# Kernel tuning notes

Hardware: AMD Instinct MI355X
Metric: run time of the kernel (lower is better)

The kernel has to match this reference:

```python
import jax, jax.numpy as jnp
import numpy as np

K = 3          # kernel_size
N = K * K      # sampling points per pixel
STRIDE = 1
PAD = 1
DIL = 1


def _conv2d(x, w, b):
    # standard NCHW conv for offset / modulation branches
    y = jax.lax.conv_general_dilated(
        x, w, window_strides=(STRIDE, STRIDE),
        padding=((PAD, PAD), (PAD, PAD)),
        rhs_dilation=(DIL, DIL),
        dimension_numbers=('NCHW', 'OIHW', 'NCHW'))
    return y + b[None, :, None, None]


def setup_inputs() -> dict:
    key = jax.random.key(0)
    ks = jax.random.split(key, 6)
    B, C, H, W, O = 8, 64, 96, 96, 64
    x = jax.random.normal(ks[0], (B, C, H, W), jnp.float32)
    # small random offset/modulation weights so sampling points are off-grid
    offset_w = jax.random.normal(ks[1], (2 * N, C, K, K), jnp.float32) * 0.01
    offset_b = jax.random.normal(ks[2], (2 * N,), jnp.float32) * 0.1
    m_w = jax.random.normal(ks[3], (N, C, K, K), jnp.float32) * 0.01
    m_b = jnp.zeros((N,), jnp.float32)
    # Conv3d(in=C, out=O, kernel=(1,1,N)) weight squeezed to [O, C, N]
    conv_w = jax.random.normal(ks[4], (O, C, N), jnp.float32) * (2.0 / (C * N)) ** 0.5
    conv_b = jnp.zeros((O,), jnp.float32)
    return dict(x=x, offset_w=offset_w, offset_b=offset_b,
                m_w=m_w, m_b=m_b, conv_w=conv_w, conv_b=conv_b)


def _deform_forward(x, offset_w, offset_b, m_w, m_b, conv_w, conv_b):
    B, C, H, W = x.shape
    offset = _conv2d(x, offset_w, offset_b)           # [B, 2n, h, w]
    m = jax.nn.sigmoid(_conv2d(x, m_w, m_b))          # [B, n, h, w]
    xp = jnp.pad(x, ((0, 0), (0, 0), (PAD, PAD), (PAD, PAD)))
    Hp, Wp = xp.shape[2], xp.shape[3]
    off = jnp.transpose(offset, (0, 2, 3, 1))         # [B, h, w, 2n]
    mod = jnp.transpose(m, (0, 2, 3, 1))              # [B, h, w, n]

    # p0: conv-center grid on the padded input; pn: kernel-tap offsets
    st = ((K - 1) // 2) * DIL
    p0_x = jnp.arange(st, Hp - (K // 2) * DIL, STRIDE, dtype=jnp.float32)  # [h]
    p0_y = jnp.arange(st, Wp - (K // 2) * DIL, STRIDE, dtype=jnp.float32)  # [w]
    r = jnp.arange(-((K - 1) // 2) * DIL, (K // 2) * DIL + 1, DIL, dtype=jnp.float32)
    pn_x, pn_y = jnp.meshgrid(r, r, indexing='ij')
    pn_x, pn_y = pn_x.reshape(N), pn_y.reshape(N)

    p_x = off[..., :N] + p0_x[None, :, None, None] + pn_x  # [B, h, w, n]
    p_y = off[..., N:] + p0_y[None, None, :, None] + pn_y

    fl_x = jnp.floor(jax.lax.stop_gradient(p_x))
    fl_y = jnp.floor(jax.lax.stop_gradient(p_y))
    q_tl_x = jnp.clip(fl_x, 0, Hp - 1).astype(jnp.int32)
    q_tl_y = jnp.clip(fl_y, 0, Wp - 1).astype(jnp.int32)
    q_br_x = jnp.clip(fl_x + 1, 0, Hp - 1).astype(jnp.int32)
    q_br_y = jnp.clip(fl_y + 1, 0, Wp - 1).astype(jnp.int32)

    pcx = jnp.clip(p_x, 0, Hp - 1)
    pcy = jnp.clip(p_y, 0, Wp - 1)

    tlx = q_tl_x.astype(pcx.dtype); tly = q_tl_y.astype(pcy.dtype)
    brx = q_br_x.astype(pcx.dtype); bry = q_br_y.astype(pcy.dtype)
    g_tl = (1 + (tlx - pcx)) * (1 + (tly - pcy))
    g_tr = (1 + (tlx - pcx)) * (1 - (bry - pcy))
    g_bl = (1 - (brx - pcx)) * (1 + (tly - pcy))
    g_br = (1 - (brx - pcx)) * (1 - (bry - pcy))

    xflat = xp.reshape(B, C, Hp * Wp)

    def gather(qx, qy):
        # per-batch gather: xf [C, Hp*Wp], idx [h, w, n] -> [C, h, w, n]
        return jax.vmap(lambda xf, i: xf[:, i])(xflat, qx * Wp + qy)

    xq_tl = gather(q_tl_x, q_tl_y)
    xq_tr = gather(q_tl_x, q_br_y)
    xq_bl = gather(q_br_x, q_tl_y)
    xq_br = gather(q_br_x, q_br_y)

    x_p = (g_tl[:, None] * xq_tl + g_tr[:, None] * xq_tr +
           g_bl[:, None] * xq_bl + g_br[:, None] * xq_br)
    x_p = x_p * mod[:, None]                           # modulation

    # Conv3d with (1,1,N) kernel == contraction over (C, N)
    out = jnp.einsum('bchwn,ocn->bohw', x_p, conv_w) + conv_b[None, :, None, None]
    return out


def reference(x, offset_w, offset_b, m_w, m_b, conv_w, conv_b):
    return _deform_forward(x, offset_w, offset_b, m_w, m_b, conv_w, conv_b)
```

## Files before the change

kernel.cpp:

```cpp
#include <hip/hip_runtime.h>
#include <hip/hip_fp16.h>
#include <cstddef>

#define B_   8
#define H_   96
#define W_   96
#define HW_  9216
#define PIX_ 73728

#define NWR    6
#define NWC    38
#define WINPX  228
#define NSLOTS 19

typedef __attribute__((ext_vector_type(8))) _Float16 halfx8;
typedef __attribute__((ext_vector_type(2))) __fp16 fp16x2_raw;
typedef __attribute__((ext_vector_type(4))) float floatx4;

#define XT_OFF   0
#define WFM_OFF  (XT_OFF + PIX_*64*2)
#define WFO_OFF  (WFM_OFF + 18*4*64*8*2)
#define WZ_OFF   (WFO_OFF + 18*2*64*8*2)

__device__ __forceinline__ unsigned pk2h(float a, float b) {
    fp16x2_raw h = __builtin_amdgcn_cvt_pkrtz(a, b);
    union { fp16x2_raw h2; unsigned u; } t; t.h2 = h; return t.u;
}
__device__ __forceinline__ halfx8 uph8(uint4 u) {
    union { uint4 u4; halfx8 h; } t; t.u4 = u; return t.h;
}
__device__ __forceinline__ halfx8 splat8(unsigned d) {
    union { unsigned u[4]; halfx8 h; } t;
    t.u[0] = d; t.u[1] = d; t.u[2] = d; t.u[3] = d; return t.h;
}
__device__ __forceinline__ void async_ld16(const void* g, void* l) {
    __builtin_amdgcn_global_load_lds((const __attribute__((address_space(1))) void*)g,
                                     (__attribute__((address_space(3))) void*)l,
                                     16, 0, 0);
}

__global__ __launch_bounds__(256) void k_transpose(const float* __restrict__ x,
                                                   unsigned short* __restrict__ xt,
                                                   const float* __restrict__ offw,
                                                   const float* __restrict__ mw,
                                                   const float* __restrict__ convw,
                                                   unsigned short* __restrict__ wfm,
                                                   unsigned short* __restrict__ wfo,
                                                   unsigned short* __restrict__ wz) {
    if (blockIdx.x >= 1152) {
        int g = (blockIdx.x - 1152) * 256 + threadIdx.x;
        if (g < 4608) {
            int lane = g & 63, mtks = g >> 6;
            int mt = mtks & 3, ks = mtks >> 2;
            int o = mt * 16 + (lane & 15), quad = lane >> 4;
            float v[8];
            #pragma unroll
            for (int j = 0; j < 8; ++j) {
                int k = ks * 32 + quad * 8 + j;
                int t = k / 64, c = k % 64;
                v[j] = convw[(size_t)(o * 64 + c) * 9 + t];
            }
            uint4 pk;
            pk.x = pk2h(v[0], v[1]); pk.y = pk2h(v[2], v[3]);
            pk.z = pk2h(v[4], v[5]); pk.w = pk2h(v[6], v[7]);
            *(uint4*)(wfm + (size_t)g * 8) = pk;
        } else if (g < 4608 + 2304) {
            int g2 = g - 4608;
            int lane = g2 & 63, mtks = g2 >> 6;
            int mt = mtks & 1, ks = mtks >> 1;
            int m = mt * 16 + (lane & 15), quad = lane >> 4;
            float v[8];
            #pragma unroll
            for (int j = 0; j < 8; ++j) {
                int k = ks * 32 + quad * 8 + j;
                int t = k / 64, c = k % 64;
                float f = 0.f;
                if (m < 18)      f = offw[(size_t)(m * 64 + c) * 9 + t];
                else if (m < 27) f = mw[(size_t)((m - 18) * 64 + c) * 9 + t];
                v[j] = f;
            }
            uint4 pk;
            pk.x = pk2h(v[0], v[1]); pk.y = pk2h(v[2], v[3]);
            pk.z = pk2h(v[4], v[5]); pk.w = pk2h(v[6], v[7]);
            *(uint4*)(wfo + (size_t)g2 * 8) = pk;
        } else if (g < 4608 + 2304 + 8) {
            uint4 z = make_uint4(0, 0, 0, 0);
            *(uint4*)(wz + (size_t)(g - 6912) * 8) = z;
        }
        return;
    }

    __shared__ float tile[64 * 65];
    int bb  = blockIdx.x / 144;
    int sp0 = (blockIdx.x % 144) * 64;
    int t = threadIdx.x;
    int s4 = (t & 15) * 4, cq = t >> 4;
    #pragma unroll
    for (int i = 0; i < 4; ++i) {
        int c = cq + 16 * i;
        float4 v = *(const float4*)&x[(size_t)(bb * 64 + c) * HW_ + sp0 + s4];
        tile[c * 65 + s4 + 0] = v.x;
        tile[c * 65 + s4 + 1] = v.y;
        tile[c * 65 + s4 + 2] = v.z;
        tile[c * 65 + s4 + 3] = v.w;
    }
    __syncthreads();
    int c8 = t & 7, sgrp = t >> 3;
    #pragma unroll
    for (int i = 0; i < 2; ++i) {
        int s2 = i * 32 + sgrp;
        uint4 pk;
        pk.x = pk2h(tile[(c8 * 8 + 0) * 65 + s2], tile[(c8 * 8 + 1) * 65 + s2]);
        pk.y = pk2h(tile[(c8 * 8 + 2) * 65 + s2], tile[(c8 * 8 + 3) * 65 + s2]);
        pk.z = pk2h(tile[(c8 * 8 + 4) * 65 + s2], tile[(c8 * 8 + 5) * 65 + s2]);
        pk.w = pk2h(tile[(c8 * 8 + 6) * 65 + s2], tile[(c8 * 8 + 7) * 65 + s2]);
        *(uint4*)(xt + (size_t)(bb * HW_ + sp0 + s2) * 64 + c8 * 8) = pk;
    }
}

__global__ __launch_bounds__(256, 4) void k_fused(const unsigned short* __restrict__ xt,
                                                  const unsigned short* __restrict__ wfo,
                                                  const unsigned short* __restrict__ wfm,
                                                  const float* __restrict__ offb,
                                                  const float* __restrict__ mb,
                                                  const float* __restrict__ convb,
                                                  const unsigned short* __restrict__ wz,
                                                  float* __restrict__ out) {
    __shared__ __align__(16) unsigned char s_win[(WINPX + NSLOTS) * 128];
    __shared__ __align__(16) unsigned char s_u[9216];
    __shared__ int s_cnt;
    float* s_off = (float*)s_u;
    unsigned char* s_meta = s_u;

    int tid = threadIdx.x;
    int w = tid >> 6, lane = tid & 63, col = lane & 15, quad = lane >> 4;
    int blk = (blockIdx.x & 7) * 144 + (blockIdx.x >> 3);
    int bb  = blk / 144;
    int rem = blk % 144;
    int hr  = (rem / 3) * 2;
    int wc  = (rem % 3) * 32;
    const unsigned short* xtb = xt + (size_t)bb * HW_ * 64;

    if (tid == 0) s_cnt = 0;
    {
        int p0  = lane >> 3;
        int cgx = (lane & 7) ^ p0;
        const unsigned short* wzp = wz + cgx * 8;
        for (int i = w; i < 29; i += 4) {
            int p = i * 8 + p0;
            int wr = p / NWC, wcl = p - wr * NWC;
            int gr = hr - 2 + wr, gc = wc - 3 + wcl;
            bool ok = (p < WINPX) && ((unsigned)gr < 96u) && ((unsigned)gc < 96u);
            const unsigned short* src = ok ? (xtb + ((size_t)(gr * 96 + gc) * 64 + cgx * 8)) : wzp;
            async_ld16(src, s_win + i * 1024);
        }
    }
    __syncthreads();

    floatx4 aoff0 = (floatx4){0.f, 0.f, 0.f, 0.f};
    floatx4 aoff1 = (floatx4){0.f, 0.f, 0.f, 0.f};
    {
        int wr_base = 2 + (w >> 1);
        int wc_base = 3 + (w & 1) * 16 + col;
        #pragma unroll
        for (int t = 0; t < 9; ++t) {
            int dh = t / 3 - 1, dw = t % 3 - 1;
            int p = (wr_base + dh) * NWC + (wc_base + dw);
            int pb = p << 7, psw = (p & 7) << 4;
            #pragma unroll
            for (int ksl = 0; ksl < 2; ++ksl) {
                int ks = t * 2 + ksl;
                halfx8 a0 = *(const halfx8*)(wfo + ((size_t)(ks * 2 + 0) * 64 + lane) * 8);
                halfx8 a1 = *(const halfx8*)(wfo + ((size_t)(ks * 2 + 1) * 64 + lane) * 8);
                uint4 bvu = *(const uint4*)(s_win + pb + ((quad * 16 + ksl * 64) ^ psw));
                halfx8 bv = uph8(bvu);
                aoff0 = __builtin_amdgcn_mfma_f32_16x16x32_f16(a0, bv, aoff0, 0, 0, 0);
                aoff1 = __builtin_amdgcn_mfma_f32_16x16x32_f16(a1, bv, aoff1, 0, 0, 0);
            }
        }
    }
    #pragma unroll
    for (int r = 0; r < 4; ++r) {
        s_off[(quad * 4 + r) * 66 + (w * 16 + col)] = aoff0[r];
        int m = 16 + quad * 4 + r;
        if (m < 27) s_off[m * 66 + (w * 16 + col)] = aoff1[r];
    }
    __syncthreads();

    float ox0, oy0, mv0, ox1, oy1, mv1, ox2 = 0.f, oy2 = 0.f, mv2 = 0.f;
    bool has2 = (tid + 512) < 576;
    {
        int px = tid & 63, n = tid >> 6;
        ox0 = s_off[n * 66 + px]        + offb[n];
        oy0 = s_off[(9 + n) * 66 + px]  + offb[9 + n];
        mv0 = s_off[(18 + n) * 66 + px] + mb[n];
    }
    {
        int id = tid + 256;
        int px = id & 63, n = id >> 6;
        ox1 = s_off[n * 66 + px]        + offb[n];
        oy1 = s_off[(9 + n) * 66 + px]  + offb[9 + n];
        mv1 = s_off[(18 + n) * 66 + px] + mb[n];
    }
    if (has2) {
        int id = tid + 512;
        int px = id & 63, n = id >> 6;
        ox2 = s_off[n * 66 + px]        + offb[n];
        oy2 = s_off[(9 + n) * 66 + px]  + offb[9 + n];
        mv2 = s_off[(18 + n) * 66 + px] + mb[n];
    }
    __syncthreads();

    auto meta_one = [&](int id, float ox, float oy, float mv) {
        int px = id & 63, n = id >> 6;
        float modv = 1.f / (1.f + __expf(-mv));
        int prow = hr + (px >> 5), pcol = wc + (px & 31);
        float pxx = ox + (float)(prow + 1) + (float)(n / 3 - 1);
        float pyy = oy + (float)(pcol + 1) + (float)(n % 3 - 1);
        float flx = floorf(pxx), fly = floorf(pyy);
        float tlxf = fminf(fmaxf(flx,       0.f), 97.f);
        float tlyf = fminf(fmaxf(fly,       0.f), 97.f);
        float brxf = fminf(fmaxf(flx + 1.f, 0.f), 97.f);
        float bryf = fminf(fmaxf(fly + 1.f, 0.f), 97.f);
        float pcx  = fminf(fmaxf(pxx, 0.f), 97.f);
        float pcy  = fminf(fmaxf(pyy, 0.f), 97.f);
        float gx0 = 1.f + tlxf - pcx;
        float gx1 = 1.f - (brxf - pcx);
        float gy0 = 1.f + tlyf - pcy;
        float gy1 = 1.f - (bryf - pcy);
        int tlx = (int)tlxf, tly = (int)tlyf, brx = (int)brxf, bry = (int)bryf;
        int   qxs[4] = {tlx, tlx, brx, brx};
        int   qys[4] = {tly, bry, tly, bry};
        float gs4[4] = {gx0 * gy0, gx0 * gy1, gx1 * gy0, gx1 * gy1};
        unsigned short si[4]; unsigned short hg[4];
        #pragma unroll
        for (int c4 = 0; c4 < 4; ++c4) {
            int qx = qxs[c4], qy = qys[c4];
            bool valid = (qx >= 1) && (qx <= 96) && (qy >= 1) && (qy <= 96);
            int gr = qx - 1, gc = qy - 1;
            int wr = gr - (hr - 2), wcl = gc - (wc - 3);
            bool inwin = ((unsigned)wr < (unsigned)NWR) && ((unsigned)wcl < (unsigned)NWC);
            unsigned short idxv; float gvf;
            if (inwin) {
                idxv = (unsigned short)(wr * NWC + wcl);
                gvf = gs4[c4] * modv;
            } else if (!valid) {
                idxv = 0; gvf = 0.f;
            } else {
                int s = atomicAdd(&s_cnt, 1);
                int gidx = gr * 96 + gc;
                if (s < NSLOTS) {
                    int ps = WINPX + s;
                    #pragma unroll
                    for (int ch = 0; ch < 8; ++ch) {
                        uint4 v = *(const uint4*)(xtb + (size_t)gidx * 64 + ch * 8);
                        *(uint4*)(s_win + (size_t)ps * 128 + ((ch ^ (ps & 7)) * 16)) = v;
                    }
                    idxv = (unsigned short)ps;
                } else {
                    idxv = (unsigned short)(0x8000u | (unsigned)gidx);
                }
                gvf = gs4[c4] * modv;
            }
            si[c4] = idxv;
            hg[c4] = __half_as_ushort(__float2half_rn(gvf));
        }
        uint4 mw4;
        mw4.x = si[0] | ((unsigned)si[1] << 16);
        mw4.y = si[2] | ((unsigned)si[3] << 16);
        mw4.z = hg[0] | ((unsigned)hg[1] << 16);
        mw4.w = hg[2] | ((unsigned)hg[3] << 16);
        *(uint4*)(s_meta + ((size_t)px * 9 + n) * 16) = mw4;
    };
    meta_one(tid,       ox0, oy0, mv0);
    meta_one(tid + 256, ox1, oy1, mv1);
    if (has2) meta_one(tid + 512, ox2, oy2, mv2);
    __syncthreads();

    int mth = w & 1, pg = w >> 1;
    floatx4 acc[2][2];
    #pragma unroll
    for (int jj = 0; jj < 2; ++jj)
        #pragma unroll
        for (int mtl = 0; mtl < 2; ++mtl) acc[jj][mtl] = (floatx4){0.f, 0.f, 0.f, 0.f};

    int qk0 = quad * 16, qk1 = quad * 16 + 64;

    #pragma unroll
    for (int n = 0; n < 9; ++n) {
        halfx8 af00 = *(const halfx8*)(wfm + ((size_t)((n * 2 + 0) * 4 + mth * 2 + 0) * 64 + lane) * 8);
        halfx8 af01 = *(const halfx8*)(wfm + ((size_t)((n * 2 + 0) * 4 + mth * 2 + 1) * 64 + lane) * 8);
        halfx8 af10 = *(const halfx8*)(wfm + ((size_t)((n * 2 + 1) * 4 + mth * 2 + 0) * 64 + lane) * 8);
        halfx8 af11 = *(const halfx8*)(wfm + ((size_t)((n * 2 + 1) * 4 + mth * 2 + 1) * 64 + lane) * 8);
        #pragma unroll
        for (int jj = 0; jj < 2; ++jj) {
            int px = pg * 32 + jj * 16 + col;
            uint4 mu = *(const uint4*)(s_meta + ((size_t)px * 9 + n) * 16);
            unsigned i0 = mu.x & 0xFFFFu, i1 = mu.x >> 16;
            unsigned i2 = mu.y & 0xFFFFu, i3 = mu.y >> 16;
            int pm0 = (i0 & 0x8000u) ? 0 : (int)i0;
            int pm1 = (i1 & 0x8000u) ? 0 : (int)i1;
            int pm2 = (i2 & 0x8000u) ? 0 : (int)i2;
            int pm3 = (i3 & 0x8000u) ? 0 : (int)i3;
            int b0 = pm0 << 7, s0 = (pm0 & 7) << 4;
            int b1 = pm1 << 7, s1 = (pm1 & 7) << 4;
            int b2 = pm2 << 7, s2 = (pm2 & 7) << 4;
            int b3 = pm3 << 7, s3 = (pm3 & 7) << 4;
            uint4 cA0 = *(const uint4*)(s_win + b0 + (qk0 ^ s0));
            uint4 cA1 = *(const uint4*)(s_win + b1 + (qk0 ^ s1));
            uint4 cA2 = *(const uint4*)(s_win + b2 + (qk0 ^ s2));
            uint4 cA3 = *(const uint4*)(s_win + b3 + (qk0 ^ s3));
            uint4 cB0 = *(const uint4*)(s_win + b0 + (qk1 ^ s0));
            uint4 cB1 = *(const uint4*)(s_win + b1 + (qk1 ^ s1));
            uint4 cB2 = *(const uint4*)(s_win + b2 + (qk1 ^ s2));
            uint4 cB3 = *(const uint4*)(s_win + b3 + (qk1 ^ s3));
            if (__any((int)((i0 | i1 | i2 | i3) & 0x8000u))) {
                if (i0 & 0x8000u) { size_t ga = (size_t)(i0 & 0x3FFFu) * 64 + quad * 8;
                    cA0 = *(const uint4*)(xtb + ga); cB0 = *(const uint4*)(xtb + ga + 32); }
                if (i1 & 0x8000u) { size_t ga = (size_t)(i1 & 0x3FFFu) * 64 + quad * 8;
                    cA1 = *(const uint4*)(xtb + ga); cB1 = *(const uint4*)(xtb + ga + 32); }
                if (i2 & 0x8000u) { size_t ga = (size_t)(i2 & 0x3FFFu) * 64 + quad * 8;
                    cA2 = *(const uint4*)(xtb + ga); cB2 = *(const uint4*)(xtb + ga + 32); }
                if (i3 & 0x8000u) { size_t ga = (size_t)(i3 & 0x3FFFu) * 64 + quad * 8;
                    cA3 = *(const uint4*)(xtb + ga); cB3 = *(const uint4*)(xtb + ga + 32); }
            }
            unsigned gl0 = (mu.z & 0xFFFFu) | (mu.z << 16);
            unsigned gl1 = (mu.z >> 16) | (mu.z & 0xFFFF0000u);
            unsigned gl2 = (mu.w & 0xFFFFu) | (mu.w << 16);
            unsigned gl3 = (mu.w >> 16) | (mu.w & 0xFFFF0000u);
            halfx8 g0 = splat8(gl0), g1 = splat8(gl1), g2 = splat8(gl2), g3 = splat8(gl3);
            halfx8 vA = uph8(cA0) * g0;
            vA += uph8(cA1) * g1; vA += uph8(cA2) * g2; vA += uph8(cA3) * g3;
            halfx8 vB = uph8(cB0) * g0;
            vB += uph8(cB1) * g1; vB += uph8(cB2) * g2; vB += uph8(cB3) * g3;
            acc[jj][0] = __builtin_amdgcn_mfma_f32_16x16x32_f16(af00, vA, acc[jj][0], 0, 0, 0);
            acc[jj][1] = __builtin_amdgcn_mfma_f32_16x16x32_f16(af01, vA, acc[jj][1], 0, 0, 0);
            acc[jj][0] = __builtin_amdgcn_mfma_f32_16x16x32_f16(af10, vB, acc[jj][0], 0, 0, 0);
            acc[jj][1] = __builtin_amdgcn_mfma_f32_16x16x32_f16(af11, vB, acc[jj][1], 0, 0, 0);
        }
    }

    int prow = hr + pg;
    #pragma unroll
    for (int mtl = 0; mtl < 2; ++mtl) {
        float4 cb4 = *(const float4*)&convb[mth * 32 + mtl * 16 + quad * 4];
        #pragma unroll
        for (int jj = 0; jj < 2; ++jj) {
            int sp = prow * 96 + wc + jj * 16 + col;
            #pragma unroll
            for (int r = 0; r < 4; ++r) {
                int o = mth * 32 + mtl * 16 + quad * 4 + r;
                float bias = (r == 0) ? cb4.x : (r == 1) ? cb4.y : (r == 2) ? cb4.z : cb4.w;
                out[(size_t)(bb * 64 + o) * HW_ + sp] = acc[jj][mtl][r] + bias;
            }
        }
    }
}

extern "C" void kernel_launch(void* const* d_in, const int* in_sizes, int n_in,
                              void* d_out, int out_size, void* d_ws, size_t ws_size,
                              hipStream_t stream) {
    const float* x     = (const float*)d_in[0];
    const float* offw  = (const float*)d_in[1];
    const float* offb  = (const float*)d_in[2];
    const float* mw    = (const float*)d_in[3];
    const float* mb    = (const float*)d_in[4];
    const float* convw = (const float*)d_in[5];
    const float* convb = (const float*)d_in[6];
    char* ws = (char*)d_ws;
    unsigned short* xt16 = (unsigned short*)(ws + XT_OFF);
    unsigned short* wfm  = (unsigned short*)(ws + WFM_OFF);
    unsigned short* wfo  = (unsigned short*)(ws + WFO_OFF);
    unsigned short* wz   = (unsigned short*)(ws + WZ_OFF);
    float* out = (float*)d_out;

    k_transpose<<<dim3(1152 + 28), dim3(256), 0, stream>>>(x, xt16, offw, mw, convw, wfm, wfo, wz);
    k_fused    <<<dim3(1152),      dim3(256), 0, stream>>>(xt16, wfo, wfm, offb, mb, convb, wz, out);
}
```

Measured before the change: 113.3 us.

## Remap warp tiling so each wave samples 16 pixels once and covers all 64 outputs

Warps previously split output channels in two halves, so each pixel's bilinear gather and interpolation from LDS was done twice, once per wave of a pair. Now each wave owns 16 distinct pixels and computes all four output-channel tiles, so every sample is gathered and interpolated exactly once. The cost is loading twice as many weight fragments per wave per tap, from global/L1, and wider dependency chains on four accumulators.

```diff
diff --git a/kernel.cpp b/kernel.cpp
--- a/kernel.cpp
+++ b/kernel.cpp
@@ -277,82 +277,71 @@
     if (has2) meta_one(tid + 512, ox2, oy2, mv2);
     __syncthreads();
 
-    int mth = w & 1, pg = w >> 1;
-    floatx4 acc[2][2];
-    #pragma unroll
-    for (int jj = 0; jj < 2; ++jj)
+    int px3 = (w >> 1) * 32 + (w & 1) * 16 + col;
+    floatx4 acc[4];
+    #pragma unroll
+    for (int mt = 0; mt < 4; ++mt) acc[mt] = (floatx4){0.f, 0.f, 0.f, 0.f};
+
+    int qk0 = quad * 16, qk1 = quad * 16 + 64;
+
+    #pragma unroll
+    for (int n = 0; n < 9; ++n) {
+        uint4 mu = *(const uint4*)(s_meta + ((size_t)px3 * 9 + n) * 16);
+        unsigned i0 = mu.x & 0xFFFFu, i1 = mu.x >> 16;
+        unsigned i2 = mu.y & 0xFFFFu, i3 = mu.y >> 16;
+        int pm0 = (i0 & 0x8000u) ? 0 : (int)i0;
+        int pm1 = (i1 & 0x8000u) ? 0 : (int)i1;
+        int pm2 = (i2 & 0x8000u) ? 0 : (int)i2;
+        int pm3 = (i3 & 0x8000u) ? 0 : (int)i3;
+        int b0 = pm0 << 7, s0 = (pm0 & 7) << 4;
+        int b1 = pm1 << 7, s1 = (pm1 & 7) << 4;
+        int b2 = pm2 << 7, s2 = (pm2 & 7) << 4;
+        int b3 = pm3 << 7, s3 = (pm3 & 7) << 4;
+        uint4 cA0 = *(const uint4*)(s_win + b0 + (qk0 ^ s0));
+        uint4 cA1 = *(const uint4*)(s_win + b1 + (qk0 ^ s1));
+        uint4 cA2 = *(const uint4*)(s_win + b2 + (qk0 ^ s2));
+        uint4 cA3 = *(const uint4*)(s_win + b3 + (qk0 ^ s3));
+        uint4 cB0 = *(const uint4*)(s_win + b0 + (qk1 ^ s0));
+        uint4 cB1 = *(const uint4*)(s_win + b1 + (qk1 ^ s1));
+        uint4 cB2 = *(const uint4*)(s_win + b2 + (qk1 ^ s2));
+        uint4 cB3 = *(const uint4*)(s_win + b3 + (qk1 ^ s3));
+        if (__any((int)((i0 | i1 | i2 | i3) & 0x8000u))) {
+            if (i0 & 0x8000u) { size_t ga = (size_t)(i0 & 0x3FFFu) * 64 + quad * 8;
+                cA0 = *(const uint4*)(xtb + ga); cB0 = *(const uint4*)(xtb + ga + 32); }
+            if (i1 & 0x8000u) { size_t ga = (size_t)(i1 & 0x3FFFu) * 64 + quad * 8;
+                cA1 = *(const uint4*)(xtb + ga); cB1 = *(const uint4*)(xtb + ga + 32); }
+            if (i2 & 0x8000u) { size_t ga = (size_t)(i2 & 0x3FFFu) * 64 + quad * 8;
+                cA2 = *(const uint4*)(xtb + ga); cB2 = *(const uint4*)(xtb + ga + 32); }
+            if (i3 & 0x8000u) { size_t ga = (size_t)(i3 & 0x3FFFu) * 64 + quad * 8;
+                cA3 = *(const uint4*)(xtb + ga); cB3 = *(const uint4*)(xtb + ga + 32); }
+        }
+        unsigned gl0 = (mu.z & 0xFFFFu) | (mu.z << 16);
+        unsigned gl1 = (mu.z >> 16) | (mu.z & 0xFFFF0000u);
+        unsigned gl2 = (mu.w & 0xFFFFu) | (mu.w << 16);
+        unsigned gl3 = (mu.w >> 16) | (mu.w & 0xFFFF0000u);
+        halfx8 g0 = splat8(gl0), g1 = splat8(gl1), g2 = splat8(gl2), g3 = splat8(gl3);
+        halfx8 vA = uph8(cA0) * g0;
+        vA += uph8(cA1) * g1; vA += uph8(cA2) * g2; vA += uph8(cA3) * g3;
+        halfx8 vB = uph8(cB0) * g0;
+        vB += uph8(cB1) * g1; vB += uph8(cB2) * g2; vB += uph8(cB3) * g3;
         #pragma unroll
-        for (int mtl = 0; mtl < 2; ++mtl) acc[jj][mtl] = (floatx4){0.f, 0.f, 0.f, 0.f};
-
-    int qk0 = quad * 16, qk1 = quad * 16 + 64;
-
-    #pragma unroll
-    for (int n = 0; n < 9; ++n) {
-        halfx8 af00 = *(const halfx8*)(wfm + ((size_t)((n * 2 + 0) * 4 + mth * 2 + 0) * 64 + lane) * 8);
-        halfx8 af01 = *(const halfx8*)(wfm + ((size_t)((n * 2 + 0) * 4 + mth * 2 + 1) * 64 + lane) * 8);
-        halfx8 af10 = *(const halfx8*)(wfm + ((size_t)((n * 2 + 1) * 4 + mth * 2 + 0) * 64 + lane) * 8);
-        halfx8 af11 = *(const halfx8*)(wfm + ((size_t)((n * 2 + 1) * 4 + mth * 2 + 1) * 64 + lane) * 8);
+        for (int mt = 0; mt < 4; ++mt) {
+            halfx8 afA = *(const halfx8*)(wfm + ((size_t)((n * 2 + 0) * 4 + mt) * 64 + lane) * 8);
+            halfx8 afB = *(const halfx8*)(wfm + ((size_t)((n * 2 + 1) * 4 + mt) * 64 + lane) * 8);
+            acc[mt] = __builtin_amdgcn_mfma_f32_16x16x32_f16(afA, vA, acc[mt], 0, 0, 0);
+            acc[mt] = __builtin_amdgcn_mfma_f32_16x16x32_f16(afB, vB, acc[mt], 0, 0, 0);
+        }
+    }
+
+    int sp = (hr + (w >> 1)) * 96 + wc + (w & 1) * 16 + col;
+    #pragma unroll
+    for (int mt = 0; mt < 4; ++mt) {
+        float4 cb4 = *(const float4*)&convb[mt * 16 + quad * 4];
         #pragma unroll
-        for (int jj = 0; jj < 2; ++jj) {
-            int px = pg * 32 + jj * 16 + col;
-            uint4 mu = *(const uint4*)(s_meta + ((size_t)px * 9 + n) * 16);
-            unsigned i0 = mu.x & 0xFFFFu, i1 = mu.x >> 16;
-            unsigned i2 = mu.y & 0xFFFFu, i3 = mu.y >> 16;
-            int pm0 = (i0 & 0x8000u) ? 0 : (int)i0;
-            int pm1 = (i1 & 0x8000u) ? 0 : (int)i1;
-            int pm2 = (i2 & 0x8000u) ? 0 : (int)i2;
-            int pm3 = (i3 & 0x8000u) ? 0 : (int)i3;
-            int b0 = pm0 << 7, s0 = (pm0 & 7) << 4;
-            int b1 = pm1 << 7, s1 = (pm1 & 7) << 4;
-            int b2 = pm2 << 7, s2 = (pm2 & 7) << 4;
-            int b3 = pm3 << 7, s3 = (pm3 & 7) << 4;
-            uint4 cA0 = *(const uint4*)(s_win + b0 + (qk0 ^ s0));
-            uint4 cA1 = *(const uint4*)(s_win + b1 + (qk0 ^ s1));
-            uint4 cA2 = *(const uint4*)(s_win + b2 + (qk0 ^ s2));
-            uint4 cA3 = *(const uint4*)(s_win + b3 + (qk0 ^ s3));
-            uint4 cB0 = *(const uint4*)(s_win + b0 + (qk1 ^ s0));
-            uint4 cB1 = *(const uint4*)(s_win + b1 + (qk1 ^ s1));
-            uint4 cB2 = *(const uint4*)(s_win + b2 + (qk1 ^ s2));
-            uint4 cB3 = *(const uint4*)(s_win + b3 + (qk1 ^ s3));
-            if (__any((int)((i0 | i1 | i2 | i3) & 0x8000u))) {
-                if (i0 & 0x8000u) { size_t ga = (size_t)(i0 & 0x3FFFu) * 64 + quad * 8;
-                    cA0 = *(const uint4*)(xtb + ga); cB0 = *(const uint4*)(xtb + ga + 32); }
-                if (i1 & 0x8000u) { size_t ga = (size_t)(i1 & 0x3FFFu) * 64 + quad * 8;
-                    cA1 = *(const uint4*)(xtb + ga); cB1 = *(const uint4*)(xtb + ga + 32); }
-                if (i2 & 0x8000u) { size_t ga = (size_t)(i2 & 0x3FFFu) * 64 + quad * 8;
-                    cA2 = *(const uint4*)(xtb + ga); cB2 = *(const uint4*)(xtb + ga + 32); }
-                if (i3 & 0x8000u) { size_t ga = (size_t)(i3 & 0x3FFFu) * 64 + quad * 8;
-                    cA3 = *(const uint4*)(xtb + ga); cB3 = *(const uint4*)(xtb + ga + 32); }
-            }
-            unsigned gl0 = (mu.z & 0xFFFFu) | (mu.z << 16);
-            unsigned gl1 = (mu.z >> 16) | (mu.z & 0xFFFF0000u);
-            unsigned gl2 = (mu.w & 0xFFFFu) | (mu.w << 16);
-            unsigned gl3 = (mu.w >> 16) | (mu.w & 0xFFFF0000u);
-            halfx8 g0 = splat8(gl0), g1 = splat8(gl1), g2 = splat8(gl2), g3 = splat8(gl3);
-            halfx8 vA = uph8(cA0) * g0;
-            vA += uph8(cA1) * g1; vA += uph8(cA2) * g2; vA += uph8(cA3) * g3;
-            halfx8 vB = uph8(cB0) * g0;
-            vB += uph8(cB1) * g1; vB += uph8(cB2) * g2; vB += uph8(cB3) * g3;
-            acc[jj][0] = __builtin_amdgcn_mfma_f32_16x16x32_f16(af00, vA, acc[jj][0], 0, 0, 0);
-            acc[jj][1] = __builtin_amdgcn_mfma_f32_16x16x32_f16(af01, vA, acc[jj][1], 0, 0, 0);
-            acc[jj][0] = __builtin_amdgcn_mfma_f32_16x16x32_f16(af10, vB, acc[jj][0], 0, 0, 0);
-            acc[jj][1] = __builtin_amdgcn_mfma_f32_16x16x32_f16(af11, vB, acc[jj][1], 0, 0, 0);
-        }
-    }
-
-    int prow = hr + pg;
-    #pragma unroll
-    for (int mtl = 0; mtl < 2; ++mtl) {
-        float4 cb4 = *(const float4*)&convb[mth * 32 + mtl * 16 + quad * 4];
-        #pragma unroll
-        for (int jj = 0; jj < 2; ++jj) {
-            int sp = prow * 96 + wc + jj * 16 + col;
-            #pragma unroll
-            for (int r = 0; r < 4; ++r) {
-                int o = mth * 32 + mtl * 16 + quad * 4 + r;
-                float bias = (r == 0) ? cb4.x : (r == 1) ? cb4.y : (r == 2) ? cb4.z : cb4.w;
-                out[(size_t)(bb * 64 + o) * HW_ + sp] = acc[jj][mtl][r] + bias;
-            }
+        for (int r = 0; r < 4; ++r) {
+            int o = mt * 16 + quad * 4 + r;
+            float bias = (r == 0) ? cb4.x : (r == 1) ? cb4.y : (r == 2) ? cb4.z : cb4.w;
+            out[(size_t)(bb * 64 + o) * HW_ + sp] = acc[mt][r] + bias;
         }
     }
 }
```

Result: faster. 109.6 us (-3.2%).
